# Optimization experiments

Hardware: AMD Instinct MI355X
Metric: run time of the kernel (lower is better)

The kernel has to match this reference:

```python
import jax, jax.numpy as jnp
import numpy as np

B, C, H, W = 8, 512, 64, 64
K = 19       # num classes (Cityscapes)
CT = 256     # transform channels


def _proj(x, w, g, b):
    # 1x1 conv (no bias) + folded eval-mode BatchNorm (per-channel scale g, bias b) + ReLU
    # x: [B,Cin,H,W], w: [Cout,Cin]
    y = jnp.einsum('bchw,oc->bohw', x, w)
    return jax.nn.relu(y * g[None, :, None, None] + b[None, :, None, None])


def setup_inputs() -> dict:
    key = jax.random.key(0)
    ks = jax.random.split(key, 12)
    s = lambda i, shape: jax.random.normal(ks[i], shape, jnp.float32) * 0.05
    ones = lambda n: jnp.ones((n,), jnp.float32)
    zeros = lambda n: jnp.zeros((n,), jnp.float32)
    return {
        'x': jax.random.normal(ks[0], (B, C, H, W), jnp.float32),
        'preds': jax.random.normal(ks[1], (B, K, H, W), jnp.float32),
        'feats_il': jax.random.normal(ks[2], (B, C, H, W), jnp.float32),
        # query_project: two 1x1 conv+BN+ReLU blocks
        'q_w1': s(3, (CT, C)), 'q_g1': ones(CT), 'q_b1': zeros(CT),
        'q_w2': s(4, (CT, CT)), 'q_g2': ones(CT), 'q_b2': zeros(CT),
        # key_project: two 1x1 conv+BN+ReLU blocks
        'k_w1': s(5, (CT, C)), 'k_g1': ones(CT), 'k_b1': zeros(CT),
        'k_w2': s(6, (CT, CT)), 'k_g2': ones(CT), 'k_b2': zeros(CT),
        # value_project: one 1x1 conv+BN+ReLU (value_out_norm=True)
        'v_w': s(7, (CT, C)), 'v_g': ones(CT), 'v_b': zeros(CT),
        # out_project: one 1x1 conv+BN+ReLU
        'o_w': s(8, (C, CT)), 'o_g': ones(C), 'o_b': zeros(C),
    }


def reference(x, preds, feats_il, q_w1, q_g1, q_b1, q_w2, q_g2, q_b2,
              k_w1, k_g1, k_b1, k_w2, k_g2, k_b2, v_w, v_g, v_b, o_w, o_g, o_b):
    b, c, h, w = x.shape
    k = preds.shape[1]
    hw = h * w
    feats = x.reshape(b, c, hw).transpose(0, 2, 1)        # [B,HW,C]
    logits = preds.reshape(b, k, hw).transpose(0, 2, 1)   # [B,HW,K]
    argmax = jnp.argmax(logits, axis=-1)                  # [B,HW]
    onehot = jax.nn.one_hot(argmax, k, dtype=x.dtype)     # [B,HW,K]
    NEG = jnp.asarray(-1e9, x.dtype)
    masked = jnp.where(onehot > 0, logits, NEG)
    # per-class softmax over the pixels assigned to that class
    wgt = jax.nn.softmax(masked, axis=1)                  # [B,HW,K]
    cls_feat = jnp.einsum('bpk,bpc->bkc', wgt, feats)     # [B,K,C]
    # scatter class descriptor back to every pixel of that class
    feats_sl = jnp.take_along_axis(cls_feat, argmax[:, :, None], axis=1)  # [B,HW,C]
    feats_sl = feats_sl.transpose(0, 2, 1).reshape(b, c, h, w)
    # SelfAttentionBlock: query from inputs, key/value from feats_sl
    q = _proj(_proj(x, q_w1, q_g1, q_b1), q_w2, q_g2, q_b2)
    kk = _proj(_proj(feats_sl, k_w1, k_g1, k_b1), k_w2, k_g2, k_b2)
    v = _proj(feats_sl, v_w, v_g, v_b)
    ct = q.shape[1]
    qf = q.reshape(b, ct, hw).transpose(0, 2, 1)          # [B,HW,CT]
    kf = kk.reshape(b, ct, hw)                            # [B,CT,HW]
    vf = v.reshape(b, ct, hw).transpose(0, 2, 1)          # [B,HW,CT]
    sim = jnp.einsum('bqc,bck->bqk', qf, kf) * (ct ** -0.5)
    attn = jax.nn.softmax(sim, axis=-1)
    ctx = jnp.einsum('bqk,bkc->bqc', attn, vf)            # [B,HW,CT]
    ctx = ctx.transpose(0, 2, 1).reshape(b, ct, h, w)
    return _proj(ctx, o_w, o_g, o_b)
```

## Files before the change

### kernel.cpp

```cpp
#include <hip/hip_runtime.h>
#include <math.h>

#define HW 4096
#define NB 8
#define NK 19
#define CIN 512
#define CTC 256

typedef __attribute__((ext_vector_type(8))) short short8;
typedef __attribute__((ext_vector_type(4))) float f32x4;

__device__ inline unsigned short f2bf(float x) {
  unsigned u = __float_as_uint(x);
  return (unsigned short)((u + 0x7fffu + ((u >> 16) & 1u)) >> 16);
}
__device__ inline float bf2f(unsigned short h) {
  return __uint_as_float(((unsigned)h) << 16);
}
__device__ inline void gload16(const void* g, void* l) {
  __builtin_amdgcn_global_load_lds(
      (const __attribute__((address_space(1))) void*)g,
      (__attribute__((address_space(3))) void*)l, 16, 0, 0);
}

__global__ __launch_bounds__(256) void wconv(
    const float* __restrict__ w1, const float* __restrict__ w2,
    const float* __restrict__ wo, unsigned short* __restrict__ wb1,
    unsigned short* __restrict__ wb2, unsigned short* __restrict__ wbo,
    uint4* __restrict__ wgtP_z, uint4* __restrict__ cls_feat_z,
    uint4* __restrict__ atom_z) {
  int gid = blockIdx.x * 256 + threadIdx.x;
  int i = gid * 4;
  const float* src;
  unsigned short* dst;
  int off;
  if (i < 131072) { src = w1; dst = wb1; off = i; }
  else if (i < 196608) { src = w2; dst = wb2; off = i - 131072; }
  else { src = wo; dst = wbo; off = i - 196608; }
  float4 v = *(const float4*)(src + off);
  dst[off + 0] = f2bf(v.x);
  dst[off + 1] = f2bf(v.y);
  dst[off + 2] = f2bf(v.z);
  dst[off + 3] = f2bf(v.w);
  uint4 z = {0u, 0u, 0u, 0u};
  for (int j = gid; j < 131072; j += 81920) wgtP_z[j] = z;
  for (int j = gid; j < 19456; j += 81920) cls_feat_z[j] = z;
  if (gid < 192) atom_z[gid] = z;
}

__global__ __launch_bounds__(256) void k1a(
    const float* __restrict__ preds, float* __restrict__ bestg,
    int* __restrict__ clsg, unsigned int* __restrict__ Mu_g,
    unsigned int* __restrict__ cnt_g) {
  int b = blockIdx.y;
  int p = blockIdx.x * 256 + threadIdx.x;
  __shared__ unsigned int Mw[NK];
  __shared__ unsigned int Cw[NK];
  int tid = threadIdx.x;
  if (tid < NK) { Mw[tid] = 0u; Cw[tid] = 0u; }
  __syncthreads();
  const float* pb = preds + (size_t)b * NK * HW;
  float best = pb[p];
  int bi = 0;
#pragma unroll
  for (int k = 1; k < NK; ++k) {
    float v = pb[k * HW + p];
    if (v > best) { best = v; bi = k; }
  }
  bestg[b * HW + p] = best;
  clsg[b * HW + p] = bi;
  unsigned fb = __float_as_uint(best);
  unsigned key = (fb & 0x80000000u) ? ~fb : (fb | 0x80000000u);
  atomicMax(&Mw[bi], key);
  atomicAdd(&Cw[bi], 1u);
  __syncthreads();
  if (tid < NK) {
    if (Mw[tid]) atomicMax(&Mu_g[b * 32 + tid], Mw[tid]);
    if (Cw[tid]) atomicAdd(&cnt_g[b * 32 + tid], Cw[tid]);
  }
}

__global__ __launch_bounds__(256) void k1b(
    float* __restrict__ bestg, const int* __restrict__ clsg,
    const unsigned int* __restrict__ Mu_g, float* __restrict__ Zf_g) {
  int b = blockIdx.y;
  int p = blockIdx.x * 256 + threadIdx.x;
  __shared__ float Mf[NK];
  __shared__ float Zw[NK];
  int tid = threadIdx.x;
  if (tid < NK) {
    unsigned key = Mu_g[b * 32 + tid];
    float m = -1e30f;
    if (key) {
      unsigned fb = (key & 0x80000000u) ? (key & 0x7fffffffu) : ~key;
      m = __uint_as_float(fb);
    }
    Mf[tid] = m;
    Zw[tid] = 0.f;
  }
  __syncthreads();
  int c = clsg[b * HW + p];
  float e = expf(bestg[b * HW + p] - Mf[c]);
  bestg[b * HW + p] = e;
  atomicAdd(&Zw[c], e);
  __syncthreads();
  if (tid < NK && Zw[tid] != 0.f) atomicAdd(&Zf_g[b * 32 + tid], Zw[tid]);
}

__global__ __launch_bounds__(256) void k1c(
    const float* __restrict__ eg, const int* __restrict__ clsg,
    const float* __restrict__ Zf_g, const unsigned int* __restrict__ cnt_g,
    unsigned short* __restrict__ wgtP, float* __restrict__ countf) {
  int b = blockIdx.y;
  int p = blockIdx.x * 256 + threadIdx.x;
  __shared__ float Zl[NK];
  int tid = threadIdx.x;
  if (tid < NK) Zl[tid] = Zf_g[b * 32 + tid];
  __syncthreads();
  int c = clsg[b * HW + p];
  wgtP[((size_t)b * 32 + c) * HW + p] = f2bf(eg[b * HW + p] / Zl[c]);
  if (blockIdx.x == 0 && tid < NK)
    countf[b * NK + tid] = (float)cnt_g[b * 32 + tid];
}

__global__ __launch_bounds__(256) void xk2(
    const float* __restrict__ x, const unsigned short* __restrict__ wgtP,
    unsigned short* __restrict__ xT, float* __restrict__ cls_feat) {
  __shared__ float tile[64][65];
  __shared__ unsigned short Bs[32 * 516];
  int b = blockIdx.z, c0 = blockIdx.y * 64, pbase = blockIdx.x * 512;
  int tid = threadIdx.x;
  int l = tid & 63, w = tid >> 6;
  {
    const unsigned short* wb =
        wgtP + ((size_t)b * 32 + (tid >> 3)) * HW + pbase;
    int cof = (tid & 7) * 8;
#pragma unroll
    for (int it = 0; it < 8; ++it)
      *(short8*)&Bs[(tid >> 3) * 516 + cof + it * 64] =
          *(const short8*)&wb[cof + it * 64];
  }
  f32x4 acc[2];
  acc[0] = (f32x4){0.f, 0.f, 0.f, 0.f};
  acc[1] = (f32x4){0.f, 0.f, 0.f, 0.f};
  int cbase = w * 16;
  for (int s = 0; s < 8; ++s) {
    int ps = pbase + s * 64;
    __syncthreads();
#pragma unroll
    for (int r = 0; r < 4; ++r) {
      int cl = r * 16 + (tid >> 4);
      int pl = (tid & 15) * 4;
      float4 v = *(const float4*)&x[((size_t)b * CIN + c0 + cl) * HW + ps + pl];
      tile[cl][pl + 0] = v.x;
      tile[cl][pl + 1] = v.y;
      tile[cl][pl + 2] = v.z;
      tile[cl][pl + 3] = v.w;
    }
    __syncthreads();
#pragma unroll
    for (int j = 0; j < 16; ++j) {
      int ploc = j * 4 + w;
      xT[((size_t)b * HW + ps + ploc) * CIN + c0 + l] = f2bf(tile[l][ploc]);
    }
#pragma unroll
    for (int ch = 0; ch < 2; ++ch) {
      int pt = ch * 32 + (l >> 4) * 8;
      union { short8 v; unsigned short u[8]; } af;
      const float* tp = &tile[cbase + (l & 15)][pt];
#pragma unroll
      for (int j = 0; j < 8; ++j) af.u[j] = f2bf(tp[j]);
      int pg = s * 64 + pt;
#pragma unroll
      for (int mf = 0; mf < 2; ++mf) {
        short8 bf = *(const short8*)&Bs[(mf * 16 + (l & 15)) * 516 + pg];
        acc[mf] =
            __builtin_amdgcn_mfma_f32_16x16x32_bf16(af.v, bf, acc[mf], 0, 0, 0);
      }
    }
  }
#pragma unroll
  for (int mf = 0; mf < 2; ++mf) {
    int k = mf * 16 + (l & 15);
    if (k < NK) {
#pragma unroll
      for (int r = 0; r < 4; ++r) {
        int c = c0 + cbase + (l >> 4) * 4 + r;
        atomicAdd(&cls_feat[((size_t)b * NK + k) * CIN + c], acc[mf][r]);
      }
    }
  }
}

__global__ __launch_bounds__(256) void k3a(
    const float* __restrict__ cls_feat, const float* __restrict__ kw1,
    const float* __restrict__ kg1, const float* __restrict__ kb1,
    const float* __restrict__ vw, const float* __restrict__ vg,
    const float* __restrict__ vb, float* __restrict__ h1g,
    float* __restrict__ Vcls) {
  int bk = blockIdx.y;
  int b = bk / NK, kc = bk % NK;
  int q = blockIdx.x;
  __shared__ float cf[CIN];
  int tid = threadIdx.x;
  const float* row = cls_feat + (size_t)bk * CIN;
  for (int i = tid; i < CIN; i += 256) cf[i] = row[i];
  __syncthreads();
  int o = tid >> 1, half = tid & 1;
  int col = q * 64 + (o & 63);
  const float* w =
      (o < 64) ? &kw1[(size_t)col * CIN] : &vw[(size_t)col * CIN];
  int base = half * 256;
  float acc[4] = {0.f, 0.f, 0.f, 0.f};
#pragma unroll 8
  for (int i = 0; i < 64; ++i) {
    float4 w4 = *(const float4*)&w[base + i * 4];
    const float* c4 = &cf[base + i * 4];
    acc[i & 3] += w4.x * c4[0] + w4.y * c4[1] + w4.z * c4[2] + w4.w * c4[3];
  }
  float s = (acc[0] + acc[1]) + (acc[2] + acc[3]);
  s += __shfl_xor(s, 1);
  if (half == 0) {
    if (o < 64) {
      h1g[(size_t)bk * CTC + col] = fmaxf(s * kg1[col] + kb1[col], 0.f);
    } else {
      Vcls[((size_t)b * CTC + col) * NK + kc] =
          fmaxf(s * vg[col] + vb[col], 0.f);
    }
  }
}

__global__ __launch_bounds__(256) void k3b(
    const float* __restrict__ h1g, const float* __restrict__ kw2,
    const float* __restrict__ kg2, const float* __restrict__ kb2,
    unsigned short* __restrict__ KclsT) {
  int bk = blockIdx.y;
  int q = blockIdx.x;
  __shared__ float h1[CTC];
  int tid = threadIdx.x;
  const float* row = h1g + (size_t)bk * CTC;
  if (tid < CTC) h1[tid] = row[tid];
  __syncthreads();
  int o = tid >> 2, part = tid & 3;
  int col = q * 64 + o;
  const float* w = &kw2[(size_t)col * CTC + part * 64];
  const float* c = &h1[part * 64];
  float acc[4] = {0.f, 0.f, 0.f, 0.f};
#pragma unroll
  for (int i = 0; i < 16; ++i) {
    float4 w4 = *(const float4*)&w[i * 4];
    acc[i & 3] += w4.x * c[i * 4] + w4.y * c[i * 4 + 1] + w4.z * c[i * 4 + 2] +
                  w4.w * c[i * 4 + 3];
  }
  float s = (acc[0] + acc[1]) + (acc[2] + acc[3]);
  s += __shfl_xor(s, 1);
  s += __shfl_xor(s, 2);
  if (part == 0)
    KclsT[(size_t)bk * CTC + col] = f2bf(fmaxf(s * kg2[col] + kb2[col], 0.f));
}

template <int KD>
__global__ __launch_bounds__(256) void gemm_mfma(
    const unsigned short* __restrict__ A, const unsigned short* __restrict__ Wb,
    const float* __restrict__ g, const float* __restrict__ bb,
    void* __restrict__ Y, int M, int outmode) {
  __shared__ __align__(16) unsigned short As[2][128 * 32];
  __shared__ __align__(16) unsigned short Bs[2][128 * 32];
  int b = blockIdx.z;
  int n0 = blockIdx.x * 128;
  int m0 = blockIdx.y * 128;
  int tid = threadIdx.x;
  int l = tid & 63, wid = tid >> 6;
  int wr = wid >> 1, wc = wid & 1;
  const unsigned short* Ab = A + (size_t)b * HW * KD;

  f32x4 acc[4][4];
#pragma unroll
  for (int i = 0; i < 4; ++i)
#pragma unroll
    for (int j = 0; j < 4; ++j) acc[i][j] = (f32x4){0.f, 0.f, 0.f, 0.f};

  const int NT = KD / 32;
  auto STAGE = [&](int buf, int t) {
    int k0 = t * 32;
#pragma unroll
    for (int q = 0; q < 2; ++q) {
      int e = q * 2048 + tid * 8;
      int rl = e >> 5, sl = (e >> 3) & 3;
      gload16(Ab + (size_t)(n0 + rl) * KD + k0 + 8 * (sl ^ ((rl >> 1) & 3)),
              &As[buf][q * 2048 + wid * 512]);
    }
#pragma unroll
    for (int q = 0; q < 2; ++q) {
      int e = q * 2048 + tid * 8;
      int rl = e >> 5, sl = (e >> 3) & 3;
      gload16(Wb + (size_t)(m0 + rl) * KD + k0 + 8 * (sl ^ ((rl >> 1) & 3)),
              &Bs[buf][q * 2048 + wid * 512]);
    }
  };
  STAGE(0, 0);
  for (int t = 0; t < NT; ++t) {
    __syncthreads();
    if (t + 1 < NT) STAGE((t + 1) & 1, t + 1);
    int cur = t & 1;
    short8 af[4], bf[4];
#pragma unroll
    for (int f = 0; f < 4; ++f) {
      int nl = wr * 64 + f * 16 + (l & 15);
      af[f] = *(const short8*)&As[cur][nl * 32 + 8 * ((l >> 4) ^ ((nl >> 1) & 3))];
      int ml = wc * 64 + f * 16 + (l & 15);
      bf[f] = *(const short8*)&Bs[cur][ml * 32 + 8 * ((l >> 4) ^ ((ml >> 1) & 3))];
    }
#pragma unroll
    for (int i = 0; i < 4; ++i)
#pragma unroll
      for (int j = 0; j < 4; ++j)
        acc[i][j] =
            __builtin_amdgcn_mfma_f32_16x16x32_bf16(af[i], bf[j], acc[i][j], 0, 0, 0);
  }
  if (outmode == 0) {
    float* Yf = (float*)Y + (size_t)b * M * HW;
#pragma unroll
    for (int j = 0; j < 4; ++j) {
      int m = m0 + wc * 64 + j * 16 + (l & 15);
      float gm = g[m], bm = bb[m];
#pragma unroll
      for (int i = 0; i < 4; ++i) {
        int n = n0 + wr * 64 + i * 16 + (l >> 4) * 4;
        float4 o;
        o.x = fmaxf(acc[i][j][0] * gm + bm, 0.f);
        o.y = fmaxf(acc[i][j][1] * gm + bm, 0.f);
        o.z = fmaxf(acc[i][j][2] * gm + bm, 0.f);
        o.w = fmaxf(acc[i][j][3] * gm + bm, 0.f);
        *(float4*)&Yf[(size_t)m * HW + n] = o;
      }
    }
  } else {
    unsigned short* Yt = (unsigned short*)Y + (size_t)b * HW * M;
#pragma unroll
    for (int j = 0; j < 4; ++j) {
      int m = m0 + wc * 64 + j * 16 + (l & 15);
      float gm = g[m], bm = bb[m];
#pragma unroll
      for (int i = 0; i < 4; ++i) {
        int n = n0 + wr * 64 + i * 16 + (l >> 4) * 4;
#pragma unroll
        for (int r = 0; r < 4; ++r)
          Yt[(size_t)(n + r) * M + m] = f2bf(fmaxf(acc[i][j][r] * gm + bm, 0.f));
      }
    }
  }
}

__global__ __launch_bounds__(256, 1) void g2k5(
    const unsigned short* __restrict__ q1T, const unsigned short* __restrict__ W2,
    const float* __restrict__ g2, const float* __restrict__ b2,
    const unsigned short* __restrict__ KclsT, const float* __restrict__ Vcls,
    const float* __restrict__ countf, unsigned short* __restrict__ ctxT) {
  __shared__ __align__(16) char RC[49152];
  __shared__ __align__(16) unsigned short Qf[8][4096];
  __shared__ __align__(16) unsigned short Kl2[32 * 32 * 8];
  __shared__ __align__(16) unsigned short Vl2[4 * 256 * 8];
  __shared__ float cntl[NK];
  unsigned short* As = (unsigned short*)RC;
  unsigned short* Bs = (unsigned short*)(RC + 16384);
  float* simT = (float*)RC;
  unsigned short* Pl = (unsigned short*)(RC + 16896);

  int b = blockIdx.y;
  int p0 = blockIdx.x * 128;
  int tid = threadIdx.x;
  int l = tid & 63, w = tid >> 6;
  const unsigned short* q1b = q1T + ((size_t)b * HW + p0) * CTC;

  for (int i = tid; i < NK * 32; i += 256) {
    int m = i >> 5, s = i & 31;
    short8 v = *(const short8*)&KclsT[((size_t)b * NK + m) * CTC + s * 8];
    *(short8*)&Kl2[(s * 32 + m) * 8] = v;
  }
  for (int i = tid; i < 4 * 256; i += 256) {
    int s = i >> 8, c = i & 255;
    union { short8 v; unsigned short u[8]; } pk;
    const float* vr = &Vcls[((size_t)b * CTC + c) * NK];
#pragma unroll
    for (int j = 0; j < 8; ++j) {
      int k = s * 8 + j;
      pk.u[j] = (k < NK) ? f2bf(vr[k]) : (unsigned short)0;
    }
    *(short8*)&Vl2[(s * 256 + c) * 8] = pk.v;
  }
  if (tid < NK) cntl[tid] = countf[b * NK + tid];

  auto STAGE_A = [&](int buf, int t) {
    int k0 = t * 32;
#pragma unroll
    for (int q = 0; q < 2; ++q) {
      int e = q * 2048 + tid * 8;
      int rl = e >> 5, sl = (e >> 3) & 3;
      gload16(q1b + (size_t)rl * CTC + k0 + 8 * (sl ^ ((rl >> 1) & 3)),
              &As[buf * 4096 + q * 2048 + w * 512]);
    }
  };
  auto STAGE_B = [&](int buf, int t) {
    int k0 = t * 32;
#pragma unroll
    for (int q = 0; q < 4; ++q) {
      int e = q * 2048 + tid * 8;
      int rl = e >> 5, sl = (e >> 3) & 3;
      gload16(W2 + (size_t)rl * CTC + k0 + 8 * (sl ^ ((rl >> 1) & 3)),
              &Bs[buf * 8192 + q * 2048 + w * 512]);
    }
  };
  f32x4 acc[2][16];
#pragma unroll
  for (int i = 0; i < 2; ++i)
#pragma unroll
    for (int j = 0; j < 16; ++j) acc[i][j] = (f32x4){0.f, 0.f, 0.f, 0.f};
  STAGE_A(0, 0);
  STAGE_B(0, 0);
  for (int t = 0; t < 8; ++t) {
    __syncthreads();
    if (t + 1 < 8) { STAGE_A((t + 1) & 1, t + 1); STAGE_B((t + 1) & 1, t + 1); }
    int cur = t & 1;
    short8 af[2];
#pragma unroll
    for (int f = 0; f < 2; ++f) {
      int nl = w * 32 + f * 16 + (l & 15);
      af[f] =
          *(const short8*)&As[cur * 4096 + nl * 32 + 8 * ((l >> 4) ^ ((nl >> 1) & 3))];
    }
#pragma unroll
    for (int mf = 0; mf < 16; ++mf) {
      int ml = mf * 16 + (l & 15);
      short8 bf =
          *(const short8*)&Bs[cur * 8192 + ml * 32 + 8 * ((l >> 4) ^ ((ml >> 1) & 3))];
      acc[0][mf] =
          __builtin_amdgcn_mfma_f32_16x16x32_bf16(af[0], bf, acc[0][mf], 0, 0, 0);
      acc[1][mf] =
          __builtin_amdgcn_mfma_f32_16x16x32_bf16(af[1], bf, acc[1][mf], 0, 0, 0);
    }
  }
#pragma unroll
  for (int mf = 0; mf < 16; ++mf) {
    int ch = mf * 16 + (l & 15);
    float gm = g2[ch], bm = b2[ch];
    int tq = ch >> 5, slot = (ch >> 3) & 3, wi = ch & 7;
#pragma unroll
    for (int i = 0; i < 2; ++i) {
#pragma unroll
      for (int r = 0; r < 4; ++r) {
        int p = w * 32 + i * 16 + (l >> 4) * 4 + r;
        Qf[tq][p * 32 + 8 * (slot ^ ((p >> 1) & 3)) + wi] =
            f2bf(fmaxf(acc[i][mf][r] * gm + bm, 0.f));
      }
    }
  }
  __syncthreads();

  f32x4 a2[2][2];
#pragma unroll
  for (int i = 0; i < 2; ++i)
#pragma unroll
    for (int j = 0; j < 2; ++j) a2[i][j] = (f32x4){0.f, 0.f, 0.f, 0.f};
  for (int t = 0; t < 8; ++t) {
    short8 aq[2], bk[2];
#pragma unroll
    for (int f = 0; f < 2; ++f) {
      int nl = w * 32 + f * 16 + (l & 15);
      aq[f] = *(const short8*)&Qf[t][nl * 32 + 8 * ((l >> 4) ^ ((nl >> 1) & 3))];
      int s = t * 4 + (l >> 4);
      int ml = f * 16 + (l & 15);
      bk[f] = *(const short8*)&Kl2[(s * 32 + ml) * 8];
    }
#pragma unroll
    for (int i = 0; i < 2; ++i)
#pragma unroll
      for (int j = 0; j < 2; ++j)
        a2[i][j] =
            __builtin_amdgcn_mfma_f32_16x16x32_bf16(aq[i], bk[j], a2[i][j], 0, 0, 0);
  }
  __syncthreads();
#pragma unroll
  for (int i = 0; i < 2; ++i)
#pragma unroll
    for (int j = 0; j < 2; ++j) {
      int m = j * 16 + (l & 15);
      if (m < NK) {
#pragma unroll
        for (int r = 0; r < 4; ++r) {
          int p = w * 32 + i * 16 + (l >> 4) * 4 + r;
          simT[p * 33 + m] = a2[i][j][r];
        }
      }
    }
  __syncthreads();
  if (tid < 128) {
    float sims[NK];
#pragma unroll
    for (int k = 0; k < NK; ++k) sims[k] = simT[tid * 33 + k] * 0.0625f;
    float m = -1e30f;
#pragma unroll
    for (int k = 0; k < NK; ++k)
      if (cntl[k] > 0.f) m = fmaxf(m, sims[k]);
    float d = 0.f;
#pragma unroll
    for (int k = 0; k < NK; ++k) {
      float e = (cntl[k] > 0.f) ? expf(sims[k] - m) : 0.f;
      sims[k] = cntl[k] * e;
      d += sims[k];
    }
    float inv = 1.f / d;
#pragma unroll
    for (int s = 0; s < 4; ++s) {
      union { short8 v; unsigned short u8[8]; } pk;
#pragma unroll
      for (int j = 0; j < 8; ++j) {
        int k = s * 8 + j;
        pk.u8[j] = (k < NK) ? f2bf(sims[k] * inv) : (unsigned short)0;
      }
      *(short8*)&Pl[(s * 128 + tid) * 8] = pk.v;
    }
  }
  __syncthreads();
  short8 ap[2];
#pragma unroll
  for (int f = 0; f < 2; ++f) {
    int nl = w * 32 + f * 16 + (l & 15);
    ap[f] = *(const short8*)&Pl[((l >> 4) * 128 + nl) * 8];
  }
  unsigned short* cb = ctxT + ((size_t)b * HW + p0) * CTC;
#pragma unroll
  for (int mc = 0; mc < 4; ++mc) {
#pragma unroll
    for (int mf = 0; mf < 4; ++mf) {
      int ml = mc * 64 + mf * 16 + (l & 15);
      short8 bv = *(const short8*)&Vl2[((l >> 4) * 256 + ml) * 8];
#pragma unroll
      for (int nf = 0; nf < 2; ++nf) {
        f32x4 z = {0.f, 0.f, 0.f, 0.f};
        f32x4 o = __builtin_amdgcn_mfma_f32_16x16x32_bf16(ap[nf], bv, z, 0, 0, 0);
#pragma unroll
        for (int r = 0; r < 4; ++r) {
          int p = w * 32 + nf * 16 + (l >> 4) * 4 + r;
          cb[(size_t)p * CTC + ml] = f2bf(o[r]);
        }
      }
    }
  }
}

extern "C" void kernel_launch(void* const* d_in, const int* in_sizes, int n_in,
                              void* d_out, int out_size, void* d_ws, size_t ws_size,
                              hipStream_t stream) {
  const float* x = (const float*)d_in[0];
  const float* preds = (const float*)d_in[1];
  const float* q_w1 = (const float*)d_in[3];
  const float* q_g1 = (const float*)d_in[4];
  const float* q_b1 = (const float*)d_in[5];
  const float* q_w2 = (const float*)d_in[6];
  const float* q_g2 = (const float*)d_in[7];
  const float* q_b2 = (const float*)d_in[8];
  const float* k_w1 = (const float*)d_in[9];
  const float* k_g1 = (const float*)d_in[10];
  const float* k_b1 = (const float*)d_in[11];
  const float* k_w2 = (const float*)d_in[12];
  const float* k_g2 = (const float*)d_in[13];
  const float* k_b2 = (const float*)d_in[14];
  const float* v_w = (const float*)d_in[15];
  const float* v_g = (const float*)d_in[16];
  const float* v_b = (const float*)d_in[17];
  const float* o_w = (const float*)d_in[18];
  const float* o_g = (const float*)d_in[19];
  const float* o_b = (const float*)d_in[20];
  float* out = (float*)d_out;

  char* base = (char*)d_ws;
  unsigned short* xT = (unsigned short*)base;
  unsigned short* q1T = (unsigned short*)(base + 33554432);
  unsigned short* ctxT = q1T;
  char* f32r = base + 50331648;
  unsigned short* wgtP = (unsigned short*)f32r;
  float* countf = (float*)(f32r + 2097152);
  float* cls_feat = (float*)(f32r + 2098176);
  unsigned short* KclsT = (unsigned short*)(f32r + 2409472);
  float* Vcls = (float*)(f32r + 2487296);
  unsigned short* wb1 = (unsigned short*)(f32r + 2642944);
  unsigned short* wb2 = (unsigned short*)(f32r + 2905088);
  unsigned short* wbo = (unsigned short*)(f32r + 3036160);
  float* h1g = (float*)(f32r + 3298304);
  float* bestg = (float*)(f32r + 3453952);
  int* clsg = (int*)(f32r + 3585024);
  unsigned int* Mu_g = (unsigned int*)(f32r + 3716096);
  unsigned int* cnt_g = (unsigned int*)(f32r + 3717120);
  float* Zf_g = (float*)(f32r + 3718144);

  wconv<<<320, 256, 0, stream>>>(q_w1, q_w2, o_w, wb1, wb2, wbo,
                                 (uint4*)wgtP, (uint4*)cls_feat, (uint4*)Mu_g);
  k1a<<<dim3(16, NB), 256, 0, stream>>>(preds, bestg, clsg, Mu_g, cnt_g);
  k1b<<<dim3(16, NB), 256, 0, stream>>>(bestg, clsg, Mu_g, Zf_g);
  k1c<<<dim3(16, NB), 256, 0, stream>>>(bestg, clsg, Zf_g, cnt_g, wgtP,
                                        countf);
  xk2<<<dim3(8, 8, NB), 256, 0, stream>>>(x, wgtP, xT, cls_feat);
  k3a<<<dim3(4, NB * NK), 256, 0, stream>>>(cls_feat, k_w1, k_g1, k_b1, v_w,
                                            v_g, v_b, h1g, Vcls);
  k3b<<<dim3(4, NB * NK), 256, 0, stream>>>(h1g, k_w2, k_g2, k_b2, KclsT);
  gemm_mfma<CIN><<<dim3(32, 2, NB), 256, 0, stream>>>(xT, wb1, q_g1, q_b1,
                                                      (void*)q1T, CTC, 1);
  g2k5<<<dim3(HW / 128, NB), 256, 0, stream>>>(q1T, wb2, q_g2, q_b2, KclsT,
                                               Vcls, countf, ctxT);
  gemm_mfma<CTC><<<dim3(32, 4, NB), 256, 0, stream>>>(ctxT, wbo, o_g, o_b,
                                                      (void*)out, CIN, 0);
}
```

Baseline: 132.6 us.

## Fuse weight conversion with argmax, drop k1c, and build class weights in xk2

Merges the weight-conversion/zeroing kernel with the per-pixel argmax kernel into a single launch. Global atomics are replaced with per-block partial buffers that consumers reduce themselves. The k1c kernel and the dense wgtP buffer, along with its zeroing, are removed, and xk2 now builds the one-hot softmax weight tile directly in LDS from bestg/clsg. This saves two launches and about 2 MB of zeroing and write/read traffic, at the cost of redundant small partial reductions in several kernels.

```diff
diff --git a/kernel.cpp b/kernel.cpp
--- a/kernel.cpp
+++ b/kernel.cpp
@@ -23,73 +23,75 @@
       (__attribute__((address_space(3))) void*)l, 16, 0, 0);
 }
 
-__global__ __launch_bounds__(256) void wconv(
+__global__ __launch_bounds__(256) void wk1a(
     const float* __restrict__ w1, const float* __restrict__ w2,
     const float* __restrict__ wo, unsigned short* __restrict__ wb1,
     unsigned short* __restrict__ wb2, unsigned short* __restrict__ wbo,
-    uint4* __restrict__ wgtP_z, uint4* __restrict__ cls_feat_z,
-    uint4* __restrict__ atom_z) {
-  int gid = blockIdx.x * 256 + threadIdx.x;
-  int i = gid * 4;
-  const float* src;
-  unsigned short* dst;
-  int off;
-  if (i < 131072) { src = w1; dst = wb1; off = i; }
-  else if (i < 196608) { src = w2; dst = wb2; off = i - 131072; }
-  else { src = wo; dst = wbo; off = i - 196608; }
-  float4 v = *(const float4*)(src + off);
-  dst[off + 0] = f2bf(v.x);
-  dst[off + 1] = f2bf(v.y);
-  dst[off + 2] = f2bf(v.z);
-  dst[off + 3] = f2bf(v.w);
-  uint4 z = {0u, 0u, 0u, 0u};
-  for (int j = gid; j < 131072; j += 81920) wgtP_z[j] = z;
-  for (int j = gid; j < 19456; j += 81920) cls_feat_z[j] = z;
-  if (gid < 192) atom_z[gid] = z;
-}
-
-__global__ __launch_bounds__(256) void k1a(
-    const float* __restrict__ preds, float* __restrict__ bestg,
-    int* __restrict__ clsg, unsigned int* __restrict__ Mu_g,
-    unsigned int* __restrict__ cnt_g) {
-  int b = blockIdx.y;
-  int p = blockIdx.x * 256 + threadIdx.x;
+    uint4* __restrict__ cls_feat_z, const float* __restrict__ preds,
+    float* __restrict__ bestg, int* __restrict__ clsg,
+    unsigned int* __restrict__ Mu_part, unsigned int* __restrict__ cnt_part) {
   __shared__ unsigned int Mw[NK];
   __shared__ unsigned int Cw[NK];
+  int bx = blockIdx.x;
   int tid = threadIdx.x;
-  if (tid < NK) { Mw[tid] = 0u; Cw[tid] = 0u; }
-  __syncthreads();
-  const float* pb = preds + (size_t)b * NK * HW;
-  float best = pb[p];
-  int bi = 0;
-#pragma unroll
-  for (int k = 1; k < NK; ++k) {
-    float v = pb[k * HW + p];
-    if (v > best) { best = v; bi = k; }
-  }
-  bestg[b * HW + p] = best;
-  clsg[b * HW + p] = bi;
-  unsigned fb = __float_as_uint(best);
-  unsigned key = (fb & 0x80000000u) ? ~fb : (fb | 0x80000000u);
-  atomicMax(&Mw[bi], key);
-  atomicAdd(&Cw[bi], 1u);
-  __syncthreads();
-  if (tid < NK) {
-    if (Mw[tid]) atomicMax(&Mu_g[b * 32 + tid], Mw[tid]);
-    if (Cw[tid]) atomicAdd(&cnt_g[b * 32 + tid], Cw[tid]);
+  if (bx < 320) {
+    int gid = bx * 256 + tid;
+    int i = gid * 4;
+    const float* src;
+    unsigned short* dst;
+    int off;
+    if (i < 131072) { src = w1; dst = wb1; off = i; }
+    else if (i < 196608) { src = w2; dst = wb2; off = i - 131072; }
+    else { src = wo; dst = wbo; off = i - 196608; }
+    float4 v = *(const float4*)(src + off);
+    dst[off + 0] = f2bf(v.x);
+    dst[off + 1] = f2bf(v.y);
+    dst[off + 2] = f2bf(v.z);
+    dst[off + 3] = f2bf(v.w);
+    uint4 z = {0u, 0u, 0u, 0u};
+    for (int j = gid; j < 19456; j += 81920) cls_feat_z[j] = z;
+  } else {
+    int bq = bx - 320;
+    int b = bq >> 4, pblk = bq & 15;
+    if (tid < NK) { Mw[tid] = 0u; Cw[tid] = 0u; }
+    __syncthreads();
+    int p = pblk * 256 + tid;
+    const float* pb = preds + (size_t)b * NK * HW;
+    float best = pb[p];
+    int bi = 0;
+#pragma unroll
+    for (int k = 1; k < NK; ++k) {
+      float v = pb[k * HW + p];
+      if (v > best) { best = v; bi = k; }
+    }
+    bestg[b * HW + p] = best;
+    clsg[b * HW + p] = bi;
+    unsigned fb = __float_as_uint(best);
+    unsigned key = (fb & 0x80000000u) ? ~fb : (fb | 0x80000000u);
+    atomicMax(&Mw[bi], key);
+    atomicAdd(&Cw[bi], 1u);
+    __syncthreads();
+    if (tid < 32) {
+      Mu_part[(b * 16 + pblk) * 32 + tid] = (tid < NK) ? Mw[tid] : 0u;
+      cnt_part[(b * 16 + pblk) * 32 + tid] = (tid < NK) ? Cw[tid] : 0u;
+    }
   }
 }
 
 __global__ __launch_bounds__(256) void k1b(
     float* __restrict__ bestg, const int* __restrict__ clsg,
-    const unsigned int* __restrict__ Mu_g, float* __restrict__ Zf_g) {
-  int b = blockIdx.y;
-  int p = blockIdx.x * 256 + threadIdx.x;
+    const unsigned int* __restrict__ Mu_part, float* __restrict__ Zf_part) {
+  int b = blockIdx.y, pblk = blockIdx.x;
+  int tid = threadIdx.x;
   __shared__ float Mf[NK];
   __shared__ float Zw[NK];
-  int tid = threadIdx.x;
   if (tid < NK) {
-    unsigned key = Mu_g[b * 32 + tid];
+    unsigned key = 0u;
+#pragma unroll
+    for (int j = 0; j < 16; ++j) {
+      unsigned v = Mu_part[(b * 16 + j) * 32 + tid];
+      key = (v > key) ? v : key;
+    }
     float m = -1e30f;
     if (key) {
       unsigned fb = (key & 0x80000000u) ? (key & 0x7fffffffu) : ~key;
@@ -99,46 +101,39 @@
     Zw[tid] = 0.f;
   }
   __syncthreads();
+  int p = pblk * 256 + tid;
   int c = clsg[b * HW + p];
   float e = expf(bestg[b * HW + p] - Mf[c]);
   bestg[b * HW + p] = e;
   atomicAdd(&Zw[c], e);
   __syncthreads();
-  if (tid < NK && Zw[tid] != 0.f) atomicAdd(&Zf_g[b * 32 + tid], Zw[tid]);
-}
-
-__global__ __launch_bounds__(256) void k1c(
-    const float* __restrict__ eg, const int* __restrict__ clsg,
-    const float* __restrict__ Zf_g, const unsigned int* __restrict__ cnt_g,
-    unsigned short* __restrict__ wgtP, float* __restrict__ countf) {
-  int b = blockIdx.y;
-  int p = blockIdx.x * 256 + threadIdx.x;
-  __shared__ float Zl[NK];
-  int tid = threadIdx.x;
-  if (tid < NK) Zl[tid] = Zf_g[b * 32 + tid];
-  __syncthreads();
-  int c = clsg[b * HW + p];
-  wgtP[((size_t)b * 32 + c) * HW + p] = f2bf(eg[b * HW + p] / Zl[c]);
-  if (blockIdx.x == 0 && tid < NK)
-    countf[b * NK + tid] = (float)cnt_g[b * 32 + tid];
+  if (tid < 32) Zf_part[(b * 16 + pblk) * 32 + tid] = (tid < NK) ? Zw[tid] : 0.f;
 }
 
 __global__ __launch_bounds__(256) void xk2(
-    const float* __restrict__ x, const unsigned short* __restrict__ wgtP,
+    const float* __restrict__ x, const float* __restrict__ eg,
+    const int* __restrict__ clsg, const float* __restrict__ Zf_part,
     unsigned short* __restrict__ xT, float* __restrict__ cls_feat) {
   __shared__ float tile[64][65];
   __shared__ unsigned short Bs[32 * 516];
+  __shared__ float Zl[NK];
   int b = blockIdx.z, c0 = blockIdx.y * 64, pbase = blockIdx.x * 512;
   int tid = threadIdx.x;
   int l = tid & 63, w = tid >> 6;
+  if (tid < NK) {
+    float s = 0.f;
+#pragma unroll
+    for (int j = 0; j < 16; ++j) s += Zf_part[(b * 16 + j) * 32 + tid];
+    Zl[tid] = s;
+  }
   {
-    const unsigned short* wb =
-        wgtP + ((size_t)b * 32 + (tid >> 3)) * HW + pbase;
-    int cof = (tid & 7) * 8;
-#pragma unroll
-    for (int it = 0; it < 8; ++it)
-      *(short8*)&Bs[(tid >> 3) * 516 + cof + it * 64] =
-          *(const short8*)&wb[cof + it * 64];
+    uint4 z = {0u, 0u, 0u, 0u};
+    for (int i = tid; i < 2064; i += 256) ((uint4*)Bs)[i] = z;
+  }
+  __syncthreads();
+  for (int i = tid; i < 512; i += 256) {
+    int c = clsg[b * HW + pbase + i];
+    Bs[c * 516 + i] = f2bf(eg[b * HW + pbase + i] / Zl[c]);
   }
   f32x4 acc[2];
   acc[0] = (f32x4){0.f, 0.f, 0.f, 0.f};
@@ -356,7 +351,7 @@
     const unsigned short* __restrict__ q1T, const unsigned short* __restrict__ W2,
     const float* __restrict__ g2, const float* __restrict__ b2,
     const unsigned short* __restrict__ KclsT, const float* __restrict__ Vcls,
-    const float* __restrict__ countf, unsigned short* __restrict__ ctxT) {
+    const unsigned int* __restrict__ cnt_part, unsigned short* __restrict__ ctxT) {
   __shared__ __align__(16) char RC[49152];
   __shared__ __align__(16) unsigned short Qf[8][4096];
   __shared__ __align__(16) unsigned short Kl2[32 * 32 * 8];
@@ -389,7 +384,12 @@
     }
     *(short8*)&Vl2[(s * 256 + c) * 8] = pk.v;
   }
-  if (tid < NK) cntl[tid] = countf[b * NK + tid];
+  if (tid < NK) {
+    unsigned int s = 0u;
+#pragma unroll
+    for (int j = 0; j < 16; ++j) s += cnt_part[(b * 16 + j) * 32 + tid];
+    cntl[tid] = (float)s;
+  }
 
   auto STAGE_A = [&](int buf, int t) {
     int k0 = t * 32;
@@ -579,35 +579,32 @@
   unsigned short* q1T = (unsigned short*)(base + 33554432);
   unsigned short* ctxT = q1T;
   char* f32r = base + 50331648;
-  unsigned short* wgtP = (unsigned short*)f32r;
-  float* countf = (float*)(f32r + 2097152);
-  float* cls_feat = (float*)(f32r + 2098176);
-  unsigned short* KclsT = (unsigned short*)(f32r + 2409472);
-  float* Vcls = (float*)(f32r + 2487296);
-  unsigned short* wb1 = (unsigned short*)(f32r + 2642944);
-  unsigned short* wb2 = (unsigned short*)(f32r + 2905088);
-  unsigned short* wbo = (unsigned short*)(f32r + 3036160);
-  float* h1g = (float*)(f32r + 3298304);
-  float* bestg = (float*)(f32r + 3453952);
-  int* clsg = (int*)(f32r + 3585024);
-  unsigned int* Mu_g = (unsigned int*)(f32r + 3716096);
-  unsigned int* cnt_g = (unsigned int*)(f32r + 3717120);
-  float* Zf_g = (float*)(f32r + 3718144);
-
-  wconv<<<320, 256, 0, stream>>>(q_w1, q_w2, o_w, wb1, wb2, wbo,
-                                 (uint4*)wgtP, (uint4*)cls_feat, (uint4*)Mu_g);
-  k1a<<<dim3(16, NB), 256, 0, stream>>>(preds, bestg, clsg, Mu_g, cnt_g);
-  k1b<<<dim3(16, NB), 256, 0, stream>>>(bestg, clsg, Mu_g, Zf_g);
-  k1c<<<dim3(16, NB), 256, 0, stream>>>(bestg, clsg, Zf_g, cnt_g, wgtP,
-                                        countf);
-  xk2<<<dim3(8, 8, NB), 256, 0, stream>>>(x, wgtP, xT, cls_feat);
+  float* cls_feat = (float*)f32r;
+  unsigned short* KclsT = (unsigned short*)(f32r + 311296);
+  float* Vcls = (float*)(f32r + 389120);
+  unsigned short* wb1 = (unsigned short*)(f32r + 544768);
+  unsigned short* wb2 = (unsigned short*)(f32r + 806912);
+  unsigned short* wbo = (unsigned short*)(f32r + 937984);
+  float* h1g = (float*)(f32r + 1200128);
+  float* bestg = (float*)(f32r + 1355776);
+  int* clsg = (int*)(f32r + 1486848);
+  unsigned int* Mu_part = (unsigned int*)(f32r + 1617920);
+  unsigned int* cnt_part = (unsigned int*)(f32r + 1634304);
+  float* Zf_part = (float*)(f32r + 1650688);
+
+  wk1a<<<448, 256, 0, stream>>>(q_w1, q_w2, o_w, wb1, wb2, wbo,
+                                (uint4*)cls_feat, preds, bestg, clsg, Mu_part,
+                                cnt_part);
+  k1b<<<dim3(16, NB), 256, 0, stream>>>(bestg, clsg, Mu_part, Zf_part);
+  xk2<<<dim3(8, 8, NB), 256, 0, stream>>>(x, bestg, clsg, Zf_part, xT,
+                                          cls_feat);
   k3a<<<dim3(4, NB * NK), 256, 0, stream>>>(cls_feat, k_w1, k_g1, k_b1, v_w,
                                             v_g, v_b, h1g, Vcls);
   k3b<<<dim3(4, NB * NK), 256, 0, stream>>>(h1g, k_w2, k_g2, k_b2, KclsT);
   gemm_mfma<CIN><<<dim3(32, 2, NB), 256, 0, stream>>>(xT, wb1, q_g1, q_b1,
                                                       (void*)q1T, CTC, 1);
   g2k5<<<dim3(HW / 128, NB), 256, 0, stream>>>(q1T, wb2, q_g2, q_b2, KclsT,
-                                               Vcls, countf, ctxT);
+                                               Vcls, cnt_part, ctxT);
   gemm_mfma<CTC><<<dim3(32, 4, NB), 256, 0, stream>>>(ctxT, wbo, o_g, o_b,
                                                       (void*)out, CIN, 0);
 }
```

Measured after the change: 127.4 us. -4.0%, faster.
